# Kernel optimization log

Hardware: AMD Instinct MI355X
Metric: run time of the kernel (lower is better)

Reference implementation:

```python
import jax, jax.numpy as jnp
import numpy as np

S, L = 512, 32            # number of sequences, max sequence length
IN_FEATURES = 13824       # 512*3*3 + 1024*3*3 ROI features
HID = 1024                # Head.hidden_dim
LSTM_H = HID // 2         # per-direction hidden size (bidirectional)
N_CLASSES = 4787
BN_EPS = 1e-5


def _make_ragged():
    lengths = (4 + (np.arange(S) % 29)).astype(np.int32)  # 4..32, sum = 9121
    n = int(lengths.sum())
    perm = np.random.RandomState(0).permutation(n).astype(np.int32)
    seq_idx = np.zeros((S, L), dtype=np.int32)
    off = 0
    for i, l in enumerate(lengths):
        seq_idx[i, :l] = perm[off:off + l]
        off += l
    return n, jnp.asarray(seq_idx), jnp.asarray(lengths)


def setup_inputs() -> dict:
    n, seq_idx, lengths = _make_ragged()
    key = jax.random.key(0)
    ks = jax.random.split(key, 16)
    w = lambda k, shp, s=0.02: (jax.random.normal(k, shp, dtype=jnp.float32) * s)
    return {
        "x": jax.random.normal(ks[0], (n, IN_FEATURES), dtype=jnp.float32),
        "fc1_w": w(ks[1], (HID, IN_FEATURES)),
        "fc1_b": w(ks[2], (HID,)),
        "bn_gamma": jnp.ones((HID,), jnp.float32),
        "bn_beta": jnp.zeros((HID,), jnp.float32),
        "fc2_w": w(ks[3], (N_CLASSES, HID)),
        "fc2_b": w(ks[4], (N_CLASSES,)),
        "w_ih_f": w(ks[5], (4 * LSTM_H, HID)),
        "w_hh_f": w(ks[6], (4 * LSTM_H, LSTM_H)),
        "b_ih_f": w(ks[7], (4 * LSTM_H,)),
        "b_hh_f": w(ks[8], (4 * LSTM_H,)),
        "w_ih_b": w(ks[9], (4 * LSTM_H, HID)),
        "w_hh_b": w(ks[10], (4 * LSTM_H, LSTM_H)),
        "b_ih_b": w(ks[11], (4 * LSTM_H,)),
        "b_hh_b": w(ks[12], (4 * LSTM_H,)),
        "seq_idx": seq_idx,
        "lengths": lengths,
    }


def _lstm_scan(seq_x, w_ih, w_hh, b_ih, b_hh):
    # seq_x: [S, L, HID] -> outputs [S, L, LSTM_H]; PyTorch gate order i,f,g,o
    s = seq_x.shape[0]
    h0 = jnp.zeros((s, LSTM_H), seq_x.dtype)
    c0 = jnp.zeros((s, LSTM_H), seq_x.dtype)
    x_gates = jnp.einsum('slh,gh->slg', seq_x, w_ih) + b_ih + b_hh  # precompute input gates

    def step(carry, xg):
        h, c = carry
        g = xg + h @ w_hh.T
        i, f, gg, o = jnp.split(g, 4, axis=-1)
        c = jax.nn.sigmoid(f) * c + jax.nn.sigmoid(i) * jnp.tanh(gg)
        h = jax.nn.sigmoid(o) * jnp.tanh(c)
        return (h, c), h

    _, hs = jax.lax.scan(step, (h0, c0), x_gates.transpose(1, 0, 2))  # [L, S, H]
    return hs.transpose(1, 0, 2)


def reference(x, fc1_w, fc1_b, bn_gamma, bn_beta, fc2_w, fc2_b,
              w_ih_f, w_hh_f, b_ih_f, b_hh_f,
              w_ih_b, w_hh_b, b_ih_b, b_hh_b,
              seq_idx, lengths):
    n = x.shape[0]
    # Head: fc1 -> relu -> BatchNorm1d (training-mode batch stats)
    h = jax.nn.relu(x @ fc1_w.T + fc1_b)
    mean = h.mean(axis=0)
    var = jnp.mean((h - mean) ** 2, axis=0)
    feats = (h - mean) * jax.lax.rsqrt(var + BN_EPS) * bn_gamma + bn_beta  # [N, HID]

    # ragged gather into packed [S, L, HID]
    mask = jnp.arange(L)[None, :] < lengths[:, None]          # [S, L]
    gidx = jnp.where(mask, seq_idx, 0)
    seq_x = feats[gidx] * mask[:, :, None]                    # zero padded slots

    # forward direction (padding at tail: harmless to causal scan)
    hf = _lstm_scan(seq_x, w_ih_f, w_hh_f, b_ih_f, b_hh_f)
    # backward direction: reverse each sequence within its valid length
    rev = jnp.clip(lengths[:, None] - 1 - jnp.arange(L)[None, :], 0, L - 1)  # [S, L]
    seq_rev = jnp.take_along_axis(seq_x, rev[:, :, None], axis=1)
    hb_rev = _lstm_scan(seq_rev, w_ih_b, w_hh_b, b_ih_b, b_hh_b)
    hb = jnp.take_along_axis(hb_rev, rev[:, :, None], axis=1)  # un-reverse (involution on valid region)

    out = jnp.concatenate([hf, hb], axis=-1)                   # [S, L, HID]

    # scatter back to flat roi order; padded slots dropped out-of-bounds
    sidx = jnp.where(mask, seq_idx, n).reshape(-1)
    lstm_feats = jnp.zeros((n, HID), feats.dtype).at[sidx].set(
        out.reshape(-1, HID), mode='drop')

    logits = lstm_feats @ fc2_w.T + fc2_b                      # apply_fc_out
    return logits
```

## Files before the change

kernel.cpp:

```cpp
#include <hip/hip_runtime.h>

typedef short short8v __attribute__((ext_vector_type(8)));
typedef float f32x4 __attribute__((ext_vector_type(4)));
typedef _Float16 h4v __attribute__((ext_vector_type(4)));

__device__ __forceinline__ unsigned short f2bf(float f){
  unsigned int u = __float_as_uint(f);
  u += 0x7fffu + ((u >> 16) & 1u);
  return (unsigned short)(u >> 16);
}
__device__ __forceinline__ float bf2f(unsigned short h){
  return __uint_as_float(((unsigned int)h) << 16);
}
union H2F { unsigned short u; _Float16 h; };
__device__ __forceinline__ float fp16f(unsigned short b){ H2F t; t.u = b; return (float)t.h; }

typedef __attribute__((address_space(1))) const unsigned int gu32;
typedef __attribute__((address_space(3))) unsigned int lu32;
__device__ __forceinline__ void gl16(const void* g, void* l){
  __builtin_amdgcn_global_load_lds((gu32*)g, (lu32*)l, 16, 0, 0);
}

template<int EPI>
__global__ __launch_bounds__(512, 2)
void gemm256(const unsigned short* __restrict__ A, const unsigned short* __restrict__ B,
             void* __restrict__ Cout, int M, int N, int K, int lda, int ldb, int ldc,
             const float* __restrict__ bias)
{
  __shared__ __align__(16) unsigned short As[2 * 2 * 256 * 32];
  __shared__ __align__(16) unsigned short Bs[2 * 2 * 256 * 32];

  const int tid = threadIdx.x;
  const int gx = gridDim.x;
  const int nwg = gx * gridDim.y;
  int dd = blockIdx.y * gx + blockIdx.x;
  int q8 = nwg >> 3, r8 = nwg & 7, xc = dd & 7, t8 = dd >> 3;
  int Lid = (xc < r8 ? xc * (q8 + 1) : r8 * (q8 + 1) + (xc - r8) * q8) + t8;
  const int bcol = (Lid % gx) * 256;
  const int brow = (Lid / gx) * 256;

  const int l = tid & 63, w = tid >> 6;
  const int wr = w >> 2;
  const int wn = w & 3;
  const int r16 = l & 15, kg = l >> 4;
  const int swz = (r16 >> 1) & 3;
  const int srow4 = l >> 2, sblk = l & 3;
  const int scol = (sblk ^ ((l >> 3) & 3)) * 8;

  const int kz = blockIdx.z * K;
  const unsigned short* Ag = A + (size_t)(brow + w * 32 + srow4) * lda + kz + scol;
  const unsigned short* Bg = B + (size_t)(bcol + w * 32 + srow4) * ldb + kz + scol;
  unsigned short* Asd = As + w * 1024;
  unsigned short* Bsd = Bs + w * 1024;

#define STA(buf, kh, kt) do { \
    gl16(Ag + (size_t)(kt) * 64 + (kh) * 32, Asd + (buf) * 16384 + (kh) * 8192); \
    gl16(Ag + (size_t)(kt) * 64 + (kh) * 32 + (size_t)16 * lda, Asd + (buf) * 16384 + (kh) * 8192 + 512); \
  } while (0)
#define STB(buf, kh, kt) do { \
    gl16(Bg + (size_t)(kt) * 64 + (kh) * 32, Bsd + (buf) * 16384 + (kh) * 8192); \
    gl16(Bg + (size_t)(kt) * 64 + (kh) * 32 + (size_t)16 * ldb, Bsd + (buf) * 16384 + (kh) * 8192 + 512); \
  } while (0)

  const unsigned short* Ard = As + (wr * 128 + r16) * 32 + ((kg ^ swz) * 8);
  const unsigned short* Brd = Bs + (wn * 64 + r16) * 32 + ((kg ^ swz) * 8);

  f32x4 acc[8][4];
  #pragma unroll
  for (int m = 0; m < 8; m++)
    #pragma unroll
    for (int nn = 0; nn < 4; nn++) { f32x4 z = {0.f, 0.f, 0.f, 0.f}; acc[m][nn] = z; }

  short8v af[4], bfr[4];

#define LDA4(c, kk, mq) { \
    _Pragma("unroll") for (int i = 0; i < 4; i++) \
      af[i] = *(const short8v*)(Ard + (c) * 16384 + (kk) * 8192 + ((mq) * 4 + i) * 512); }
#define LDB4(c, kk) { \
    _Pragma("unroll") for (int nn = 0; nn < 4; nn++) \
      bfr[nn] = *(const short8v*)(Brd + (c) * 16384 + (kk) * 8192 + nn * 512); }
#define MFMAQ(mq) { \
    __builtin_amdgcn_s_setprio(1); \
    _Pragma("unroll") for (int i = 0; i < 4; i++) { \
      _Pragma("unroll") for (int nn = 0; nn < 4; nn++) \
        acc[(mq) * 4 + i][nn] = __builtin_amdgcn_mfma_f32_16x16x32_bf16(af[i], bfr[nn], acc[(mq) * 4 + i][nn], 0, 0, 0); \
    } \
    __builtin_amdgcn_s_setprio(0); }

  const int nk = K >> 6;
  STA(0, 0, 0); STB(0, 0, 0); STA(0, 1, 0); STB(0, 1, 0);
  asm volatile("s_waitcnt vmcnt(4)" ::: "memory");
  __builtin_amdgcn_s_barrier();
  __builtin_amdgcn_sched_barrier(0);

  for (int j = 0; j < nk; j++) {
    const int c = j & 1, nb = c ^ 1;
    const bool pf = (j + 1 < nk);
    LDB4(c, 0); LDA4(c, 0, 0);
    if (pf) { STA(nb, 0, j + 1); STB(nb, 0, j + 1); }
    __builtin_amdgcn_s_barrier();
    MFMAQ(0);
    __builtin_amdgcn_s_barrier();
    LDA4(c, 0, 1);
    if (pf) { STA(nb, 1, j + 1); STB(nb, 1, j + 1); }
    __builtin_amdgcn_s_barrier();
    MFMAQ(1);
    if (pf) asm volatile("s_waitcnt vmcnt(8)" ::: "memory");
    else    asm volatile("s_waitcnt vmcnt(0)" ::: "memory");
    __builtin_amdgcn_s_barrier();
    __builtin_amdgcn_sched_barrier(0);
    LDB4(c, 1); LDA4(c, 1, 0);
    __builtin_amdgcn_s_barrier();
    MFMAQ(0);
    __builtin_amdgcn_s_barrier();
    LDA4(c, 1, 1);
    __builtin_amdgcn_s_barrier();
    MFMAQ(1);
    if (pf) asm volatile("s_waitcnt vmcnt(4)" ::: "memory");
    __builtin_amdgcn_s_barrier();
    __builtin_amdgcn_sched_barrier(0);
  }
#undef STA
#undef STB
#undef LDA4
#undef LDB4
#undef MFMAQ

  #pragma unroll
  for (int m = 0; m < 8; m++) {
    const int row0 = brow + wr * 128 + m * 16 + kg * 4;
    #pragma unroll
    for (int nn = 0; nn < 4; nn++) {
      const int col = bcol + wn * 64 + nn * 16 + r16;
      if (col < N) {
        const float bv = (EPI == 5) ? 0.f : bias[col];
        #pragma unroll
        for (int rr = 0; rr < 4; rr++) {
          const int row = row0 + rr;
          if (row < M) {
            float val = acc[m][nn][rr] + bv;
            if (EPI == 3) {
              int dL = col >> 11, rc = col & 2047;
              int cg = rc >> 6, g = (rc >> 4) & 3, u = rc & 15;
              int pc = (dL << 11) + (((cg << 4) + u) << 2) + g;
              ((_Float16*)Cout)[(size_t)row * ldc + pc] = (_Float16)val;
            } else if (EPI == 5) {
              ((_Float16*)Cout)[(size_t)blockIdx.z * M * ldc + (size_t)row * ldc + col] = (_Float16)val;
            } else {
              ((float*)Cout)[(size_t)row * ldc + col] = val;
            }
          }
        }
      }
    }
  }
}

__global__ __launch_bounds__(256) void fc1_reduce(const _Float16* __restrict__ P, const float* __restrict__ bias,
                                                  unsigned short* __restrict__ h, float* __restrict__ part,
                                                  int n, int mpad) {
  int b = blockIdx.x, tid = threadIdx.x;
  int c0 = tid * 4;
  float4 bsv = *(const float4*)(bias + c0);
  float s[4] = {0,0,0,0}, qq[4] = {0,0,0,0};
  int rbeg = b * 32;
  for (int r = rbeg; r < rbeg + 32; r++) {
    h4v a0 = *(const h4v*)(P + (size_t)r * 1024 + c0);
    h4v a1 = *(const h4v*)(P + ((size_t)mpad + r) * 1024 + c0);
    h4v a2 = *(const h4v*)(P + ((size_t)2 * mpad + r) * 1024 + c0);
    float v0 = fmaxf((float)a0[0] + (float)a1[0] + (float)a2[0] + bsv.x, 0.f);
    float v1 = fmaxf((float)a0[1] + (float)a1[1] + (float)a2[1] + bsv.y, 0.f);
    float v2 = fmaxf((float)a0[2] + (float)a1[2] + (float)a2[2] + bsv.z, 0.f);
    float v3 = fmaxf((float)a0[3] + (float)a1[3] + (float)a2[3] + bsv.w, 0.f);
    if (r < n) {
      s[0] += v0; qq[0] += v0 * v0;
      s[1] += v1; qq[1] += v1 * v1;
      s[2] += v2; qq[2] += v2 * v2;
      s[3] += v3; qq[3] += v3 * v3;
    }
    *(ushort4*)(h + (size_t)r * 1024 + c0) = make_ushort4(f2bf(v0), f2bf(v1), f2bf(v2), f2bf(v3));
  }
  float* pp = part + (size_t)b * 2048;
  #pragma unroll
  for (int k = 0; k < 4; k++) { pp[(c0 + k) * 2] = s[k]; pp[(c0 + k) * 2 + 1] = qq[k]; }
}

__global__ __launch_bounds__(256, 1)
void lstm_persist(const unsigned short* __restrict__ whhc, const unsigned short* __restrict__ bcp,
                  const _Float16* __restrict__ G,
                  const int* __restrict__ gf, const int* __restrict__ gb, const int* __restrict__ sb,
                  unsigned short* __restrict__ hst,
                  unsigned short* __restrict__ lfeat, int* __restrict__ flags)
{
  __shared__ __align__(16) unsigned short Bsh[128 * 512];
  const int tid = threadIdx.x;
  const int l = tid & 63, w = tid >> 6;
  const int b = blockIdx.x;
  const int grp = b & 15;
  const int c = b >> 4;
  const int d = grp >> 3;
  const int rowbase = d * 512 + (grp & 7) * 64;
  const int r16 = l & 15, kg = l >> 4;
  const int swzl = (r16 & 7) * 8;
  const int hu0 = c * 32 + r16;

  const unsigned short* Bsrc = whhc + ((size_t)(d * 2048 + c * 128)) * 512;
  #pragma unroll
  for (int i = 0; i < 32; i++) {
    int rr = w * 32 + i;
    gl16(Bsrc + (size_t)rr * 512 + ((l * 8) ^ ((rr & 7) * 8)), Bsh + rr * 512);
  }
  asm volatile("s_waitcnt vmcnt(0)");
  __syncthreads();

  float creg[2][4];
  #pragma unroll
  for (int m = 0; m < 2; m++)
    #pragma unroll
    for (int rr = 0; rr < 4; rr++) creg[m][rr] = 0.f;

  for (int t = 0; t < 32; t++) {
    ushort4 gv[2][4];
    int scv[4];
    #pragma unroll
    for (int rr = 0; rr < 4; rr++) {
      int row = rowbase + w * 16 + kg * 4 + rr;
      int sq = row & 511;
      int gi = d ? gb[sq * 32 + t] : gf[sq * 32 + t];
      const unsigned short* src = (gi >= 0)
          ? (const unsigned short*)G + ((size_t)gi * 4096 + (d << 11))
          : bcp + (d << 11);
      gv[0][rr] = *(const ushort4*)(src + hu0 * 4);
      gv[1][rr] = *(const ushort4*)(src + (hu0 + 16) * 4);
      scv[rr] = d ? sb[sq * 32 + t] : gi;
    }

    if (t > 0) {
      while (true) {
        int fv = 0x7fffffff;
        if (l < 16)
          fv = __hip_atomic_load(flags + ((grp * 16 + l) << 5), __ATOMIC_RELAXED, __HIP_MEMORY_SCOPE_AGENT);
        if (__all(fv >= t)) break;
        __builtin_amdgcn_s_sleep(1);
      }
    }
    asm volatile("" ::: "memory");

    const unsigned short* hp = hst + (size_t)(t & 1) * (1024 * 512);
    unsigned short* hn = hst + (size_t)((t + 1) & 1) * (1024 * 512);

    short8v av[16];
    {
      unsigned long long a64 = (unsigned long long)(hp + (size_t)(rowbase + w * 16 + r16) * 512 + kg * 8);
      #pragma unroll
      for (int kf = 0; kf < 16; kf++) {
        asm volatile("global_load_dwordx4 %0, %1, off offset:%c2 sc0 sc1"
                     : "=v"(av[kf]) : "v"(a64), "i"(kf * 64) : "memory");
      }
    }
    asm volatile("s_waitcnt vmcnt(0)" ::: "memory");

    f32x4 acc[8];
    #pragma unroll
    for (int nn = 0; nn < 8; nn++) { f32x4 z = {0.f, 0.f, 0.f, 0.f}; acc[nn] = z; }

    #pragma unroll
    for (int kc = 0; kc < 8; kc++) {
      short8v bv[8][2];
      #pragma unroll
      for (int nn = 0; nn < 8; nn++)
        #pragma unroll
        for (int kk = 0; kk < 2; kk++)
          bv[nn][kk] = *(const short8v*)(Bsh + (nn * 16 + r16) * 512 + ((kc * 64 + kk * 32 + kg * 8) ^ swzl));
      #pragma unroll
      for (int kk = 0; kk < 2; kk++)
        #pragma unroll
        for (int nn = 0; nn < 8; nn++)
          acc[nn] = __builtin_amdgcn_mfma_f32_16x16x32_bf16(av[kc * 2 + kk], bv[nn][kk], acc[nn], 0, 0, 0);
    }

    #pragma unroll
    for (int cgl = 0; cgl < 2; cgl++) {
      const int hu = hu0 + cgl * 16;
      #pragma unroll
      for (int reg = 0; reg < 4; reg++) {
        int row = rowbase + w * 16 + kg * 4 + reg;
        float g_i = acc[cgl * 4 + 0][reg] + fp16f(gv[cgl][reg].x);
        float g_f = acc[cgl * 4 + 1][reg] + fp16f(gv[cgl][reg].y);
        float g_g = acc[cgl * 4 + 2][reg] + fp16f(gv[cgl][reg].z);
        float g_o = acc[cgl * 4 + 3][reg] + fp16f(gv[cgl][reg].w);
        float si = 1.f / (1.f + __expf(-g_i));
        float sf = 1.f / (1.f + __expf(-g_f));
        float so = 1.f / (1.f + __expf(-g_o));
        float cn = sf * creg[cgl][reg] + si * tanhf(g_g);
        float hnv = so * tanhf(cn);
        creg[cgl][reg] = cn;
        unsigned int hb = f2bf(hnv);
        unsigned long long ha = (unsigned long long)(hn + (size_t)row * 512 + hu);
        asm volatile("global_store_short %0, %1, off sc0 sc1" :: "v"(ha), "v"(hb) : "memory");
        int sc = scv[reg];
        if (sc >= 0) lfeat[(size_t)sc * 1024 + d * 512 + hu] = f2bf(hnv);
      }
    }

    __syncthreads();
    if (t < 31 && tid == 0)
      __hip_atomic_store(flags + ((grp * 16 + c) << 5), t + 1, __ATOMIC_RELAXED, __HIP_MEMORY_SCOPE_AGENT);
  }
}

__global__ __launch_bounds__(256) void conv_bf16(const float* __restrict__ src, unsigned short* __restrict__ dst,
                                                 size_t nvalid, size_t total) {
  size_t stride = (size_t)gridDim.x * 2048;
  for (size_t i = ((size_t)blockIdx.x * 256 + threadIdx.x) * 8; i < total; i += stride) {
    unsigned short o[8];
    if (i + 8 <= nvalid) {
      float4 a = *(const float4*)(src + i);
      float4 b = *(const float4*)(src + i + 4);
      o[0] = f2bf(a.x); o[1] = f2bf(a.y); o[2] = f2bf(a.z); o[3] = f2bf(a.w);
      o[4] = f2bf(b.x); o[5] = f2bf(b.y); o[6] = f2bf(b.z); o[7] = f2bf(b.w);
    } else {
      #pragma unroll
      for (int j = 0; j < 8; j++) o[j] = (i + j < nvalid) ? f2bf(src[i + j]) : (unsigned short)0;
    }
    *(ushort4*)(dst + i) = make_ushort4(o[0], o[1], o[2], o[3]);
    *(ushort4*)(dst + i + 4) = make_ushort4(o[4], o[5], o[6], o[7]);
  }
}

__global__ __launch_bounds__(256) void bn_final(const float* __restrict__ part, const float* __restrict__ gamma,
                                                const float* __restrict__ beta, float* __restrict__ scale,
                                                float* __restrict__ shift, int M, int nb) {
  int c = blockIdx.x * 256 + threadIdx.x;
  float s = 0.f, q = 0.f;
  for (int b = 0; b < nb; b++) { s += part[(size_t)b * 2048 + c * 2]; q += part[(size_t)b * 2048 + c * 2 + 1]; }
  float mean = s / (float)M;
  float var = q / (float)M - mean * mean;
  float sc = gamma[c] * rsqrtf(var + 1e-5f);
  scale[c] = sc; shift[c] = beta[c] - mean * sc;
}

__global__ __launch_bounds__(256) void prep_tables(const int* __restrict__ seq_idx, const int* __restrict__ lengths,
                                                   int* __restrict__ gf, int* __restrict__ gb, int* __restrict__ sb) {
  int idx = blockIdx.x * 256 + threadIdx.x;
  if (idx < 512 * 32) {
    int s = idx >> 5, t = idx & 31;
    int len = lengths[s];
    gf[idx] = (t < len) ? seq_idx[idx] : -1;
    int rb = len - 1 - t;
    gb[idx] = seq_idx[(s << 5) + (rb < 0 ? 0 : rb)];
    sb[idx] = (t < len) ? seq_idx[(s << 5) + (len - 1 - t)] : -1;
  }
}

__global__ __launch_bounds__(256) void build_wih(const float* __restrict__ wf, const float* __restrict__ wb,
                                                 const float* __restrict__ bihf, const float* __restrict__ bhhf,
                                                 const float* __restrict__ bihb, const float* __restrict__ bhhb,
                                                 const float* __restrict__ scale, const float* __restrict__ shift,
                                                 unsigned short* __restrict__ wcdst, float* __restrict__ bc,
                                                 _Float16* __restrict__ bcp) {
  int orow = blockIdx.x * 4 + (threadIdx.x >> 6);
  int l = threadIdx.x & 63;
  int dir = orow >> 11, j = orow & 2047;
  int cc = j >> 6, jj = j & 63, g = jj >> 4, u = jj & 15;
  int srow = g * 512 + cc * 16 + u;
  const float* src = (dir ? wb : wf) + (size_t)srow * 1024;
  unsigned short* dst = wcdst + (size_t)orow * 1024;
  float sacc = 0.f;
  #pragma unroll
  for (int jv = 0; jv < 16; jv++) {
    int k = l + jv * 64;
    float v = src[k];
    sacc += shift[k] * v;
    dst[k] = f2bf(v * scale[k]);
  }
  #pragma unroll
  for (int o2 = 32; o2 > 0; o2 >>= 1) sacc += __shfl_down(sacc, o2);
  if (l == 0) {
    float bb = (dir ? (bihb[srow] + bhhb[srow]) : (bihf[srow] + bhhf[srow])) + sacc;
    bc[orow] = bb;
    int pc = (dir << 11) + (((cc << 4) + u) << 2) + g;
    bcp[pc] = (_Float16)bb;
  }
}

__global__ __launch_bounds__(256) void build_whh(const float* __restrict__ wf, const float* __restrict__ wb,
                                                 unsigned short* __restrict__ o) {
  int cidx = blockIdx.x * 256 + threadIdx.x;
  if (cidx < 4096 * 64) {
    int orow = cidx >> 6, k0 = (cidx & 63) * 8;
    int dir = orow >> 11, j = orow & 2047;
    int cc = j >> 7, L = j & 127;
    int cgl = L >> 6, g = (L >> 4) & 3, u = L & 15;
    int hunit = cc * 32 + cgl * 16 + u;
    const float* src = (dir ? wb : wf) + (size_t)(g * 512 + hunit) * 512 + k0;
    unsigned short* dst = o + (size_t)orow * 512 + k0;
    float4 a = *(const float4*)(src);
    float4 bq = *(const float4*)(src + 4);
    dst[0] = f2bf(a.x); dst[1] = f2bf(a.y); dst[2] = f2bf(a.z); dst[3] = f2bf(a.w);
    dst[4] = f2bf(bq.x); dst[5] = f2bf(bq.y); dst[6] = f2bf(bq.z); dst[7] = f2bf(bq.w);
  }
}

extern "C" void kernel_launch(void* const* d_in, const int* in_sizes, int n_in,
                              void* d_out, int out_size, void* d_ws, size_t ws_size,
                              hipStream_t stream) {
  const float* x     = (const float*)d_in[0];
  const float* fc1w  = (const float*)d_in[1];
  const float* fc1b  = (const float*)d_in[2];
  const float* gamma = (const float*)d_in[3];
  const float* beta  = (const float*)d_in[4];
  const float* fc2w  = (const float*)d_in[5];
  const float* fc2b  = (const float*)d_in[6];
  const float* wihf  = (const float*)d_in[7];
  const float* whhf  = (const float*)d_in[8];
  const float* bihf  = (const float*)d_in[9];
  const float* bhhf  = (const float*)d_in[10];
  const float* wihb  = (const float*)d_in[11];
  const float* whhb  = (const float*)d_in[12];
  const float* bihb  = (const float*)d_in[13];
  const float* bhhb  = (const float*)d_in[14];
  const int* seq_idx = (const int*)d_in[15];
  const int* lengths = (const int*)d_in[16];
  float* out = (float*)d_out;

  const int n = in_sizes[0] / 13824;
  const int mt = (n + 255) / 256;
  const int mpad = mt * 256;

  char* ws = (char*)d_ws;
  size_t off = 0;
  auto alloc = [&](size_t bytes) -> void* {
    void* p = ws + off; off += (bytes + 255) & ~(size_t)255; return p;
  };
  unsigned short* x_h  = (unsigned short*)alloc((size_t)mpad * 13824 * 2);
  unsigned short* w1_h = (unsigned short*)alloc((size_t)1024 * 13824 * 2);
  unsigned short* w2_h = (unsigned short*)alloc((size_t)4864 * 1024 * 2);
  unsigned short* h    = (unsigned short*)alloc((size_t)mpad * 1024 * 2);
  _Float16*       G    = (_Float16*)alloc((size_t)mpad * 4096 * 2);
  unsigned short* wihc = (unsigned short*)alloc((size_t)4096 * 1024 * 2);
  unsigned short* whhc = (unsigned short*)alloc((size_t)4096 * 512 * 2);
  float* bias_c = (float*)alloc(4096 * 4);
  _Float16* bias_p = (_Float16*)alloc(4096 * 2);
  unsigned short* lfeat  = (unsigned short*)alloc((size_t)mpad * 1024 * 2);
  unsigned short* hstate = (unsigned short*)alloc((size_t)2 * 1024 * 512 * 2);
  float* part   = (float*)alloc((size_t)(mpad / 32) * 2048 * 4);
  float* scale  = (float*)alloc(1024 * 4);
  float* shift  = (float*)alloc(1024 * 4);
  int* gf  = (int*)alloc(16384 * 4);
  int* gb  = (int*)alloc(16384 * 4);
  int* sb  = (int*)alloc(16384 * 4);
  int* flags = (int*)alloc(256 * 32 * 4);

  _Float16* P16 = (_Float16*)G;

  dim3 blk(256);
  dim3 blk5(512);

  conv_bf16<<<2048, blk, 0, stream>>>(x, x_h, (size_t)n * 13824, (size_t)mpad * 13824);
  conv_bf16<<<1024, blk, 0, stream>>>(fc1w, w1_h, (size_t)1024 * 13824, (size_t)1024 * 13824);
  conv_bf16<<<256, blk, 0, stream>>>(fc2w, w2_h, (size_t)4787 * 1024, (size_t)4864 * 1024);
  build_whh<<<1024, blk, 0, stream>>>(whhf, whhb, whhc);
  prep_tables<<<64, blk, 0, stream>>>(seq_idx, lengths, gf, gb, sb);
  hipMemsetAsync(hstate, 0, (size_t)2 * 1024 * 512 * 2, stream);
  hipMemsetAsync(flags, 0, 256 * 32 * 4, stream);

  gemm256<5><<<dim3(4, mt, 3), blk5, 0, stream>>>(
      x_h, w1_h, P16, mpad, 1024, 4608, 13824, 13824, 1024, nullptr);

  fc1_reduce<<<mpad / 32, blk, 0, stream>>>(P16, fc1b, h, part, n, mpad);
  bn_final<<<4, blk, 0, stream>>>(part, gamma, beta, scale, shift, n, mpad / 32);
  build_wih<<<1024, blk, 0, stream>>>(wihf, wihb, bihf, bhhf, bihb, bhhb, scale, shift, wihc, bias_c, bias_p);

  gemm256<3><<<dim3(16, mt), blk5, 0, stream>>>(
      h, wihc, G, n, 4096, 1024, 1024, 1024, 4096, bias_c);

  lstm_persist<<<256, blk, 0, stream>>>(whhc, (const unsigned short*)bias_p, G, gf, gb, sb,
                                        hstate, lfeat, flags);

  gemm256<0><<<dim3(19, mt), blk5, 0, stream>>>(
      lfeat, w2_h, out, n, 4787, 1024, 1024, 1024, 4787, fc2b);
}
```

Before: 1.237 ms.

## Store LSTM hidden state in fragment-ordered layout and rebalance GEMM prefetch stages

The recurrent LSTM kernel now writes the bf16 hidden state in a layout that matches the MFMA A-fragment order. Each wave's per-step reads become contiguous 1 KB chunks instead of strided row reads, and the stores use immediate offsets from one base address. Separately, the GEMM main loop spreads its next-tile A and B global-to-LDS prefetches over four sub-phases instead of two, with adjusted vmcnt waits, to smooth memory issue against MFMA work. The layout change depends on every producer and consumer of the hidden-state buffer agreeing on the new indexing, and the reworked waitcnt values must still cover the outstanding loads.

```diff
diff --git a/kernel.cpp b/kernel.cpp
--- a/kernel.cpp
+++ b/kernel.cpp
@@ -97,23 +97,25 @@
     const int c = j & 1, nb = c ^ 1;
     const bool pf = (j + 1 < nk);
     LDB4(c, 0); LDA4(c, 0, 0);
-    if (pf) { STA(nb, 0, j + 1); STB(nb, 0, j + 1); }
+    if (pf) STA(nb, 0, j + 1);
     __builtin_amdgcn_s_barrier();
     MFMAQ(0);
     __builtin_amdgcn_s_barrier();
     LDA4(c, 0, 1);
-    if (pf) { STA(nb, 1, j + 1); STB(nb, 1, j + 1); }
+    if (pf) STB(nb, 0, j + 1);
     __builtin_amdgcn_s_barrier();
     MFMAQ(1);
-    if (pf) asm volatile("s_waitcnt vmcnt(8)" ::: "memory");
+    if (pf) asm volatile("s_waitcnt vmcnt(4)" ::: "memory");
     else    asm volatile("s_waitcnt vmcnt(0)" ::: "memory");
     __builtin_amdgcn_s_barrier();
     __builtin_amdgcn_sched_barrier(0);
     LDB4(c, 1); LDA4(c, 1, 0);
+    if (pf) STA(nb, 1, j + 1);
     __builtin_amdgcn_s_barrier();
     MFMAQ(0);
     __builtin_amdgcn_s_barrier();
     LDA4(c, 1, 1);
+    if (pf) STB(nb, 1, j + 1);
     __builtin_amdgcn_s_barrier();
     MFMAQ(1);
     if (pf) asm volatile("s_waitcnt vmcnt(4)" ::: "memory");
@@ -219,6 +221,9 @@
     #pragma unroll
     for (int rr = 0; rr < 4; rr++) creg[m][rr] = 0.f;
 
+  const size_t stbase = (size_t)(((grp * 4 + w) * 16 + c) * 4 + (r16 >> 3)) * 128 + (size_t)kg * 32 + (r16 & 7);
+  const size_t ldbase = ((size_t)(grp * 64 + w * 16) * 1024) + (size_t)l * 16;
+
   for (int t = 0; t < 32; t++) {
     ushort4 gv[2][4];
     int scv[4];
@@ -246,16 +251,24 @@
     }
     asm volatile("" ::: "memory");
 
-    const unsigned short* hp = hst + (size_t)(t & 1) * (1024 * 512);
-    unsigned short* hn = hst + (size_t)((t + 1) & 1) * (1024 * 512);
+    const unsigned short* hp = hst + (size_t)(t & 1) * 524288;
+    unsigned short* hn = hst + (size_t)((t + 1) & 1) * 524288;
 
     short8v av[16];
     {
-      unsigned long long a64 = (unsigned long long)(hp + (size_t)(rowbase + w * 16 + r16) * 512 + kg * 8);
+      unsigned long long a64 = (unsigned long long)hp * 1 + (unsigned long long)((const char*)0);
+      a64 = (unsigned long long)((const char*)hp + ldbase);
       #pragma unroll
-      for (int kf = 0; kf < 16; kf++) {
-        asm volatile("global_load_dwordx4 %0, %1, off offset:%c2 sc0 sc1"
-                     : "=v"(av[kf]) : "v"(a64), "i"(kf * 64) : "memory");
+      for (int kq = 0; kq < 4; kq++) {
+        unsigned long long aq = a64 + (unsigned long long)kq * 4096;
+        asm volatile("global_load_dwordx4 %0, %1, off offset:0 sc0 sc1"
+                     : "=v"(av[kq * 4 + 0]) : "v"(aq) : "memory");
+        asm volatile("global_load_dwordx4 %0, %1, off offset:1024 sc0 sc1"
+                     : "=v"(av[kq * 4 + 1]) : "v"(aq) : "memory");
+        asm volatile("global_load_dwordx4 %0, %1, off offset:2048 sc0 sc1"
+                     : "=v"(av[kq * 4 + 2]) : "v"(aq) : "memory");
+        asm volatile("global_load_dwordx4 %0, %1, off offset:3072 sc0 sc1"
+                     : "=v"(av[kq * 4 + 3]) : "v"(aq) : "memory");
       }
     }
     asm volatile("s_waitcnt vmcnt(0)" ::: "memory");
@@ -279,6 +292,7 @@
           acc[nn] = __builtin_amdgcn_mfma_f32_16x16x32_bf16(av[kc * 2 + kk], bv[nn][kk], acc[nn], 0, 0, 0);
     }
 
+    unsigned long long ha = (unsigned long long)((char*)hn + stbase * 2);
     #pragma unroll
     for (int cgl = 0; cgl < 2; cgl++) {
       const int hu = hu0 + cgl * 16;
@@ -296,8 +310,17 @@
         float hnv = so * tanhf(cn);
         creg[cgl][reg] = cn;
         unsigned int hb = f2bf(hnv);
-        unsigned long long ha = (unsigned long long)(hn + (size_t)row * 512 + hu);
-        asm volatile("global_store_short %0, %1, off sc0 sc1" :: "v"(ha), "v"(hb) : "memory");
+        if (cgl == 0) {
+          if (reg == 0) asm volatile("global_store_short %0, %1, off offset:0 sc0 sc1" :: "v"(ha), "v"(hb) : "memory");
+          if (reg == 1) asm volatile("global_store_short %0, %1, off offset:16 sc0 sc1" :: "v"(ha), "v"(hb) : "memory");
+          if (reg == 2) asm volatile("global_store_short %0, %1, off offset:32 sc0 sc1" :: "v"(ha), "v"(hb) : "memory");
+          if (reg == 3) asm volatile("global_store_short %0, %1, off offset:48 sc0 sc1" :: "v"(ha), "v"(hb) : "memory");
+        } else {
+          if (reg == 0) asm volatile("global_store_short %0, %1, off offset:512 sc0 sc1" :: "v"(ha), "v"(hb) : "memory");
+          if (reg == 1) asm volatile("global_store_short %0, %1, off offset:528 sc0 sc1" :: "v"(ha), "v"(hb) : "memory");
+          if (reg == 2) asm volatile("global_store_short %0, %1, off offset:544 sc0 sc1" :: "v"(ha), "v"(hb) : "memory");
+          if (reg == 3) asm volatile("global_store_short %0, %1, off offset:560 sc0 sc1" :: "v"(ha), "v"(hb) : "memory");
+        }
         int sc = scv[reg];
         if (sc >= 0) lfeat[(size_t)sc * 1024 + d * 512 + hu] = f2bf(hnv);
       }
```

New measurement: 1.135 ms. 8.3% less time.
